# Optimization experiments

Measured on AMD Instinct MI355X. Metric: run time of the kernel, lower is better.

The kernel has to match this reference:

```python
import jax, jax.numpy as jnp
import numpy as np

B, T, C, HS = 4, 4096, 1024, 64

def setup_inputs() -> dict:
    key = jax.random.key(0)
    kx, kq, kk, kv = jax.random.split(key, 4)
    x = jax.random.normal(kx, (B, T, C), dtype=jnp.float32)
    s = 1.0 / np.sqrt(C)
    Wq = jax.random.normal(kq, (C, HS), dtype=jnp.float32) * s
    Wk = jax.random.normal(kk, (C, HS), dtype=jnp.float32) * s
    Wv = jax.random.normal(kv, (C, HS), dtype=jnp.float32) * s
    return {"x": x, "Wq": Wq, "Wk": Wk, "Wv": Wv}

def reference(x, Wq, Wk, Wv):
    # q,k,v: [B,T,HS]
    q = jnp.einsum('btc,ch->bth', x, Wq)
    k = jnp.einsum('btc,ch,->bth', x, Wk) if False else jnp.einsum('btc,ch->bth', x, Wk)
    v = jnp.einsum('btc,ch->bth', x, Wv)
    dk = q.shape[-1]
    wei = jnp.einsum('bth,bsh->bts', q, k) * (dk ** -0.5)  # [B,T,T]
    Tq = wei.shape[1]
    causal = jnp.tril(jnp.ones((Tq, Tq), dtype=bool))
    wei = jnp.where(causal, wei, -jnp.inf)
    wei = jax.nn.softmax(wei, axis=-1)
    out = jnp.einsum('bts,bsh->bth', wei, v)  # [B,T,HS]
    return out
```

## Files before the change

### kernel.cpp

```cpp
#include <hip/hip_runtime.h>
#include <stdint.h>

typedef __attribute__((ext_vector_type(8))) short short8v;
typedef __attribute__((ext_vector_type(4))) float float4v;

__device__ __forceinline__ unsigned short f32_to_bf16(float f) {
    union { float f; uint32_t u; } v; v.f = f;
    uint32_t u = v.u;
    u += 0x7FFFu + ((u >> 16) & 1u);
    return (unsigned short)(u >> 16);
}

#define T_LEN 4096
#define C_DIM 1024
#define HSZ 64

__global__ void wt_kernel(const float* __restrict__ Wq, const float* __restrict__ Wk,
                          const float* __restrict__ Wv, unsigned short* __restrict__ Wtp) {
    int idx = blockIdx.x * blockDim.x + threadIdx.x;
    int e    = idx & 7;
    int lane = (idx >> 3) & 63;
    int ks   = (idx >> 9) & 31;
    int ct   = idx >> 14;
    int g = lane >> 4, c = lane & 15;
    int k   = ks * 32 + g * 8 + e;
    int col = (ct & 3) * 16 + c;
    int m   = ct >> 2;
    const float* W = (m == 0) ? Wq : ((m == 1) ? Wk : Wv);
    Wtp[idx] = f32_to_bf16(W[(size_t)k * 64 + col]);
}

#define XCH 264

__global__ __launch_bounds__(256) void qkv_kernel(
    const float* __restrict__ x, const unsigned short* __restrict__ Wtp,
    unsigned short* __restrict__ qo, unsigned short* __restrict__ kp,
    unsigned short* __restrict__ vp)
{
    __shared__ __align__(16) unsigned short xs2[2][16 * XCH];
    const int tid = threadIdx.x;
    const int bid = (int)blockIdx.x;
    const int rowidx = (((bid >> 1) & 3) << 8) + ((bid >> 3) << 1) + (bid & 1);
    const int row0 = rowidx * 16;

    const int wave = tid >> 6, lane = tid & 63;
    const int g = lane >> 4, c = lane & 15;

    const int lrow = tid >> 6;
    float4 ld[4];

    auto LOADX = [&](int cs) {
        #pragma unroll
        for (int i = 0; i < 4; ++i) {
            int f = i * 256 + tid;
            int row = f >> 6, c4 = f & 63;
            ld[i] = *((const float4*)x + (size_t)(row0 + row) * 256 + cs * 64 + c4);
        }
    };
    auto WRITEX = [&](int buf) {
        #pragma unroll
        for (int i = 0; i < 4; ++i) {
            int f = i * 256 + tid;
            int row = f >> 6, c4 = f & 63;
            union { unsigned short s[4]; uint64_t u; } pk;
            pk.s[0] = f32_to_bf16(ld[i].x); pk.s[1] = f32_to_bf16(ld[i].y);
            pk.s[2] = f32_to_bf16(ld[i].z); pk.s[3] = f32_to_bf16(ld[i].w);
            *(uint64_t*)(&xs2[buf][row * XCH + c4 * 4]) = pk.u;
        }
    };
    (void)lrow;

    LOADX(0);
    WRITEX(0);
    __syncthreads();

    float4v acc0 = {0,0,0,0}, acc1 = {0,0,0,0}, acc2 = {0,0,0,0};
    const unsigned short* wp0 = Wtp + (size_t)((wave * 3 + 0) * 32) * 512 + lane * 8;
    const unsigned short* wp1 = Wtp + (size_t)((wave * 3 + 1) * 32) * 512 + lane * 8;
    const unsigned short* wp2 = Wtp + (size_t)((wave * 3 + 2) * 32) * 512 + lane * 8;

    for (int cs = 0; cs < 4; ++cs) {
        if (cs < 3) LOADX(cs + 1);
        const int buf = cs & 1;
        #pragma unroll
        for (int k8 = 0; k8 < 8; ++k8) {
            const int ks = cs * 8 + k8;
            short8v a  = *(const short8v*)(&xs2[buf][c * XCH + k8 * 32 + g * 8]);
            short8v b0 = *(const short8v*)(wp0 + ks * 512);
            short8v b1 = *(const short8v*)(wp1 + ks * 512);
            short8v b2 = *(const short8v*)(wp2 + ks * 512);
            acc0 = __builtin_amdgcn_mfma_f32_16x16x32_bf16(a, b0, acc0, 0, 0, 0);
            acc1 = __builtin_amdgcn_mfma_f32_16x16x32_bf16(a, b1, acc1, 0, 0, 0);
            acc2 = __builtin_amdgcn_mfma_f32_16x16x32_bf16(a, b2, acc2, 0, 0, 0);
        }
        if (cs < 3) {
            __syncthreads();
            WRITEX(buf ^ 1);
            __syncthreads();
        }
    }

    float4v accs[3] = {acc0, acc1, acc2};
    #pragma unroll
    for (int t = 0; t < 3; ++t) {
        int ct = wave * 3 + t;
        int m = ct >> 2, hcol = (ct & 3) * 16 + c;
        if (m == 2) {
            const int r0 = row0 + g * 4;
            const int b  = r0 >> 12;
            const int s0_ = r0 & 4095;
            const int t2h = s0_ >> 5;
            const int gv  = (s0_ >> 3) & 3;
            const int e0  = s0_ & 7;
            union { unsigned short s[4]; uint64_t u; } pk;
            #pragma unroll
            for (int j = 0; j < 4; ++j) pk.s[j] = f32_to_bf16(accs[t][j]);
            *(uint64_t*)(vp + (size_t)b * 262144 + t2h * 2048 + (ct & 3) * 512
                            + (gv * 16 + c) * 8 + e0) = pk.u;
        } else if (m == 1) {
            const int fbase = ((row0 & 4095) >> 6) * 8 + (((row0 & 4095) >> 4) & 3) * 2 + (hcol >> 5);
            const int b = row0 >> 12;
            unsigned short* kb = kp + (size_t)b * 262144 + (size_t)fbase * 512
                                 + (((hcol >> 3) & 3) * 16) * 8 + (hcol & 7);
            #pragma unroll
            for (int j = 0; j < 4; ++j)
                kb[(g * 4 + j) * 8] = f32_to_bf16(accs[t][j]);
        } else {
            float sc = 0.125f;
            #pragma unroll
            for (int j = 0; j < 4; ++j)
                qo[(size_t)(row0 + g * 4 + j) * 64 + hcol] = f32_to_bf16(accs[t][j] * sc);
        }
    }
}

#define PLD 72

__global__ __launch_bounds__(512) void attn_kernel(
    const unsigned short* __restrict__ qi, const unsigned short* __restrict__ kp,
    const unsigned short* __restrict__ vp, float* __restrict__ out)
{
    __shared__ __align__(16) unsigned short Ps[8][16 * PLD];
    __shared__ float CombO[6][16][64];
    __shared__ float CombM[6][16];
    __shared__ float CombL[6][16];

    const int tid   = threadIdx.x;
    const int wave  = tid >> 6, lane = tid & 63;
    const int qh    = wave & 1, slice = wave >> 1;
    const int g = lane >> 4, c = lane & 15;

    const int bid   = (int)blockIdx.x;
    const int batch = (bid >> 1) & 3;
    const int q0    = bid & 1;
    const int m_    = bid >> 3;
    const int mm    = m_ & 31;
    const int qb = q0 ? ((m_ < 32) ? 2 * mm + 1 : 126 - 2 * mm)
                      : ((m_ < 32) ? 2 * mm     : 127 - 2 * mm);

    const int rbase = qb * 32 + qh * 16;
    const size_t bo  = (size_t)batch * T_LEN * HSZ;
    const size_t bov = (size_t)batch * 262144;

    short8v qf0 = *(const short8v*)(qi + bo + (size_t)(rbase + c) * 64 +  0 + g * 8);
    short8v qf1 = *(const short8v*)(qi + bo + (size_t)(rbase + c) * 64 + 32 + g * 8);

    float4v acc[4];
    #pragma unroll
    for (int i2 = 0; i2 < 4; ++i2) acc[i2] = (float4v){0,0,0,0};
    float mrow = -3e38f;
    float lsum = 0.f;

    const int nt_w = ((rbase + 15) >> 6) + 1;
    unsigned short* Pw = &Ps[wave][0];

    short8v kf[8], kn[8];

    auto TILE = [&](int t, const short8v* kb) {
        const int s0 = t * 64;

        float4v sa[4];
        #pragma unroll
        for (int ct = 0; ct < 4; ++ct) {
            float4v z = {0, 0, 0, 0};
            z = __builtin_amdgcn_mfma_f32_16x16x32_bf16(kb[ct * 2 + 0], qf0, z, 0, 0, 0);
            sa[ct] = __builtin_amdgcn_mfma_f32_16x16x32_bf16(kb[ct * 2 + 1], qf1, z, 0, 0, 0);
        }

        short8v vf0[4];
        #pragma unroll
        for (int dt = 0; dt < 4; ++dt)
            vf0[dt] = *(const short8v*)(vp + bov + (size_t)(t * 8 + dt) * 512 + lane * 8);

        if (s0 + 63 > rbase) {
            #pragma unroll
            for (int ct = 0; ct < 4; ++ct)
                #pragma unroll
                for (int j = 0; j < 4; ++j)
                    if (s0 + ct * 16 + g * 4 + j > rbase + c) sa[ct][j] = -3e38f;
        }

        float mx01 = fmaxf(fmaxf(sa[0][0], sa[0][1]), fmaxf(sa[0][2], sa[0][3]));
        float mx11 = fmaxf(fmaxf(sa[1][0], sa[1][1]), fmaxf(sa[1][2], sa[1][3]));
        float mx21 = fmaxf(fmaxf(sa[2][0], sa[2][1]), fmaxf(sa[2][2], sa[2][3]));
        float mx31 = fmaxf(fmaxf(sa[3][0], sa[3][1]), fmaxf(sa[3][2], sa[3][3]));
        float mx = fmaxf(fmaxf(mx01, mx11), fmaxf(mx21, mx31));
        mx = fmaxf(mx, __shfl_xor(mx, 16, 64));
        mx = fmaxf(mx, __shfl_xor(mx, 32, 64));
        const float nm = fmaxf(mrow, mx);
        const float al = __expf(mrow - nm);
        mrow = nm;
        float ps = 0.f;
        #pragma unroll
        for (int ct = 0; ct < 4; ++ct)
            #pragma unroll
            for (int j = 0; j < 4; ++j) {
                float p = __expf(sa[ct][j] - nm);
                sa[ct][j] = p;
                ps += p;
            }
        lsum = lsum * al + ps;
        #pragma unroll
        for (int dt = 0; dt < 4; ++dt)
            #pragma unroll
            for (int j = 0; j < 4; ++j) acc[dt][j] *= al;

        #pragma unroll
        for (int ct = 0; ct < 4; ++ct) {
            union { unsigned short s[4]; uint64_t u; } pk4;
            #pragma unroll
            for (int j = 0; j < 4; ++j) pk4.s[j] = f32_to_bf16(sa[ct][j]);
            *(uint64_t*)(&Pw[c * PLD + ct * 16 + g * 4]) = pk4.u;
        }

        short8v vf1[4];
        #pragma unroll
        for (int dt = 0; dt < 4; ++dt)
            vf1[dt] = *(const short8v*)(vp + bov + (size_t)(t * 8 + 4 + dt) * 512 + lane * 8);

        short8v pa0 = *(const short8v*)(&Pw[c * PLD +  0 + g * 8]);
        short8v pa1 = *(const short8v*)(&Pw[c * PLD + 32 + g * 8]);

        #pragma unroll
        for (int dt = 0; dt < 4; ++dt)
            acc[dt] = __builtin_amdgcn_mfma_f32_16x16x32_bf16(vf0[dt], pa0, acc[dt], 0, 0, 0);
        #pragma unroll
        for (int dt = 0; dt < 4; ++dt)
            acc[dt] = __builtin_amdgcn_mfma_f32_16x16x32_bf16(vf1[dt], pa1, acc[dt], 0, 0, 0);
    };

    auto LOADK = [&](int t, short8v* kd) {
        #pragma unroll
        for (int f = 0; f < 8; ++f)
            kd[f] = *(const short8v*)(kp + bov + (size_t)(t * 8 + f) * 512 + lane * 8);
    };

    int t = slice;
    if (t < nt_w) {
        LOADK(t, kf);
        while (true) {
            const bool h1 = (t + 4 < nt_w);
            if (h1) LOADK(t + 4, kn);
            TILE(t, kf);
            if (!h1) break;
            t += 4;
            const bool h2 = (t + 4 < nt_w);
            if (h2) LOADK(t + 4, kf);
            TILE(t, kn);
            if (!h2) break;
            t += 4;
        }
    }

    lsum += __shfl_xor(lsum, 16, 64);
    lsum += __shfl_xor(lsum, 32, 64);

    if (slice > 0) {
        const int sidx = (slice - 1) * 2 + qh;
        #pragma unroll
        for (int dt = 0; dt < 4; ++dt)
            #pragma unroll
            for (int j = 0; j < 4; ++j)
                CombO[sidx][c][dt * 16 + g * 4 + j] = acc[dt][j];
        if (g == 0) {
            CombM[sidx][c] = mrow;
            CombL[sidx][c] = lsum;
        }
    }
    __syncthreads();

    if (slice == 0) {
        float M = mrow;
        #pragma unroll
        for (int s = 0; s < 3; ++s) M = fmaxf(M, CombM[s * 2 + qh][c]);
        const float a0 = __expf(mrow - M);
        float as[3];
        float lt = lsum * a0;
        #pragma unroll
        for (int s = 0; s < 3; ++s) {
            as[s] = __expf(CombM[s * 2 + qh][c] - M);
            lt += as[s] * CombL[s * 2 + qh][c];
        }
        const float linv = 1.0f / lt;
        #pragma unroll
        for (int dt = 0; dt < 4; ++dt) {
            float4 o;
            float* op = &o.x;
            #pragma unroll
            for (int j = 0; j < 4; ++j) {
                float v = acc[dt][j] * a0;
                #pragma unroll
                for (int s = 0; s < 3; ++s)
                    v += as[s] * CombO[s * 2 + qh][c][dt * 16 + g * 4 + j];
                op[j] = v * linv;
            }
            *(float4*)(out + bo + (size_t)(rbase + c) * 64 + dt * 16 + g * 4) = o;
        }
    }
}

extern "C" void kernel_launch(void* const* d_in, const int* in_sizes, int n_in,
                              void* d_out, int out_size, void* d_ws, size_t ws_size,
                              hipStream_t stream) {
    const float* x  = (const float*)d_in[0];
    const float* Wq = (const float*)d_in[1];
    const float* Wk = (const float*)d_in[2];
    const float* Wv = (const float*)d_in[3];

    unsigned short* Wt = (unsigned short*)d_ws;
    unsigned short* q  = (unsigned short*)((char*)d_ws + (size_t)3 * 65536 * 2);
    unsigned short* kp = q + (size_t)4 * T_LEN * HSZ;
    unsigned short* vp = kp + (size_t)4 * T_LEN * HSZ;
    float* out = (float*)d_out;

    hipLaunchKernelGGL(wt_kernel,  dim3(768), dim3(256), 0, stream, Wq, Wk, Wv, Wt);
    hipLaunchKernelGGL(qkv_kernel, dim3(1024), dim3(256), 0, stream, x, Wt, q, kp, vp);
    hipLaunchKernelGGL(attn_kernel, dim3(512), dim3(512), 0, stream, q, kp, vp, out);
}
```

Measured before the change: 57.83 us.

## Double QKV row tile per block and split K across wave halves

The QKV projection kernel now processes 32 rows per block with 512 threads instead of 16 rows with 256 threads. Each wave computes two 16-row tiles, so every weight fragment loaded is reused twice. The K dimension is split between two wave groups, and their partial sums are reduced through shared memory. This halves the grid and cuts redundant weight loads, at the cost of extra LDS, a reduction step with added barriers, and fewer blocks to spread across CUs.

```diff
diff --git a/kernel.cpp b/kernel.cpp
--- a/kernel.cpp
+++ b/kernel.cpp
@@ -32,27 +32,31 @@
 
 #define XCH 264
 
-__global__ __launch_bounds__(256) void qkv_kernel(
+__global__ __launch_bounds__(512) void qkv_kernel(
     const float* __restrict__ x, const unsigned short* __restrict__ Wtp,
     unsigned short* __restrict__ qo, unsigned short* __restrict__ kp,
     unsigned short* __restrict__ vp)
 {
-    __shared__ __align__(16) unsigned short xs2[2][16 * XCH];
+    __shared__ __align__(16) unsigned short xs2[2][32 * XCH];
+    __shared__ float part[4][2][3][64][4];
+
     const int tid = threadIdx.x;
     const int bid = (int)blockIdx.x;
-    const int rowidx = (((bid >> 1) & 3) << 8) + ((bid >> 3) << 1) + (bid & 1);
-    const int row0 = rowidx * 16;
+    const int batch = (bid >> 1) & 3;
+    const int q0    = bid & 1;
+    const int hi    = bid >> 3;
+    const int rg    = hi * 2 + q0;
+    const int row0  = batch * 4096 + rg * 32;
 
     const int wave = tid >> 6, lane = tid & 63;
+    const int wq = wave & 3, wh = wave >> 2;
     const int g = lane >> 4, c = lane & 15;
 
-    const int lrow = tid >> 6;
     float4 ld[4];
-
     auto LOADX = [&](int cs) {
         #pragma unroll
         for (int i = 0; i < 4; ++i) {
-            int f = i * 256 + tid;
+            int f = i * 512 + tid;
             int row = f >> 6, c4 = f & 63;
             ld[i] = *((const float4*)x + (size_t)(row0 + row) * 256 + cs * 64 + c4);
         }
@@ -60,7 +64,7 @@
     auto WRITEX = [&](int buf) {
         #pragma unroll
         for (int i = 0; i < 4; ++i) {
-            int f = i * 256 + tid;
+            int f = i * 512 + tid;
             int row = f >> 6, c4 = f & 63;
             union { unsigned short s[4]; uint64_t u; } pk;
             pk.s[0] = f32_to_bf16(ld[i].x); pk.s[1] = f32_to_bf16(ld[i].y);
@@ -68,30 +72,40 @@
             *(uint64_t*)(&xs2[buf][row * XCH + c4 * 4]) = pk.u;
         }
     };
-    (void)lrow;
 
     LOADX(0);
     WRITEX(0);
     __syncthreads();
 
-    float4v acc0 = {0,0,0,0}, acc1 = {0,0,0,0}, acc2 = {0,0,0,0};
-    const unsigned short* wp0 = Wtp + (size_t)((wave * 3 + 0) * 32) * 512 + lane * 8;
-    const unsigned short* wp1 = Wtp + (size_t)((wave * 3 + 1) * 32) * 512 + lane * 8;
-    const unsigned short* wp2 = Wtp + (size_t)((wave * 3 + 2) * 32) * 512 + lane * 8;
+    float4v acc[2][3];
+    #pragma unroll
+    for (int rt = 0; rt < 2; ++rt)
+        #pragma unroll
+        for (int t = 0; t < 3; ++t) acc[rt][t] = (float4v){0,0,0,0};
+
+    const unsigned short* wp0 = Wtp + (size_t)((wq * 3 + 0) * 32) * 512 + lane * 8;
+    const unsigned short* wp1 = Wtp + (size_t)((wq * 3 + 1) * 32) * 512 + lane * 8;
+    const unsigned short* wp2 = Wtp + (size_t)((wq * 3 + 2) * 32) * 512 + lane * 8;
 
     for (int cs = 0; cs < 4; ++cs) {
         if (cs < 3) LOADX(cs + 1);
         const int buf = cs & 1;
         #pragma unroll
-        for (int k8 = 0; k8 < 8; ++k8) {
-            const int ks = cs * 8 + k8;
-            short8v a  = *(const short8v*)(&xs2[buf][c * XCH + k8 * 32 + g * 8]);
-            short8v b0 = *(const short8v*)(wp0 + ks * 512);
-            short8v b1 = *(const short8v*)(wp1 + ks * 512);
-            short8v b2 = *(const short8v*)(wp2 + ks * 512);
-            acc0 = __builtin_amdgcn_mfma_f32_16x16x32_bf16(a, b0, acc0, 0, 0, 0);
-            acc1 = __builtin_amdgcn_mfma_f32_16x16x32_bf16(a, b1, acc1, 0, 0, 0);
-            acc2 = __builtin_amdgcn_mfma_f32_16x16x32_bf16(a, b2, acc2, 0, 0, 0);
+        for (int ksi = 0; ksi < 4; ++ksi) {
+            const int kc = 2 * ksi + wh;
+            const int ks = cs * 8 + kc;
+            const int koff = kc * 32 + g * 8;
+            short8v a0 = *(const short8v*)(&xs2[buf][(0 * 16 + c) * XCH + koff]);
+            short8v a1 = *(const short8v*)(&xs2[buf][(1 * 16 + c) * XCH + koff]);
+            short8v b0 = *(const short8v*)(wp0 + (size_t)ks * 512);
+            short8v b1 = *(const short8v*)(wp1 + (size_t)ks * 512);
+            short8v b2 = *(const short8v*)(wp2 + (size_t)ks * 512);
+            acc[0][0] = __builtin_amdgcn_mfma_f32_16x16x32_bf16(a0, b0, acc[0][0], 0, 0, 0);
+            acc[0][1] = __builtin_amdgcn_mfma_f32_16x16x32_bf16(a0, b1, acc[0][1], 0, 0, 0);
+            acc[0][2] = __builtin_amdgcn_mfma_f32_16x16x32_bf16(a0, b2, acc[0][2], 0, 0, 0);
+            acc[1][0] = __builtin_amdgcn_mfma_f32_16x16x32_bf16(a1, b0, acc[1][0], 0, 0, 0);
+            acc[1][1] = __builtin_amdgcn_mfma_f32_16x16x32_bf16(a1, b1, acc[1][1], 0, 0, 0);
+            acc[1][2] = __builtin_amdgcn_mfma_f32_16x16x32_bf16(a1, b2, acc[1][2], 0, 0, 0);
         }
         if (cs < 3) {
             __syncthreads();
@@ -100,36 +114,55 @@
         }
     }
 
-    float4v accs[3] = {acc0, acc1, acc2};
-    #pragma unroll
-    for (int t = 0; t < 3; ++t) {
-        int ct = wave * 3 + t;
-        int m = ct >> 2, hcol = (ct & 3) * 16 + c;
-        if (m == 2) {
-            const int r0 = row0 + g * 4;
-            const int b  = r0 >> 12;
-            const int s0_ = r0 & 4095;
-            const int t2h = s0_ >> 5;
-            const int gv  = (s0_ >> 3) & 3;
-            const int e0  = s0_ & 7;
-            union { unsigned short s[4]; uint64_t u; } pk;
-            #pragma unroll
-            for (int j = 0; j < 4; ++j) pk.s[j] = f32_to_bf16(accs[t][j]);
-            *(uint64_t*)(vp + (size_t)b * 262144 + t2h * 2048 + (ct & 3) * 512
-                            + (gv * 16 + c) * 8 + e0) = pk.u;
-        } else if (m == 1) {
-            const int fbase = ((row0 & 4095) >> 6) * 8 + (((row0 & 4095) >> 4) & 3) * 2 + (hcol >> 5);
-            const int b = row0 >> 12;
-            unsigned short* kb = kp + (size_t)b * 262144 + (size_t)fbase * 512
-                                 + (((hcol >> 3) & 3) * 16) * 8 + (hcol & 7);
-            #pragma unroll
-            for (int j = 0; j < 4; ++j)
-                kb[(g * 4 + j) * 8] = f32_to_bf16(accs[t][j]);
-        } else {
-            float sc = 0.125f;
-            #pragma unroll
-            for (int j = 0; j < 4; ++j)
-                qo[(size_t)(row0 + g * 4 + j) * 64 + hcol] = f32_to_bf16(accs[t][j] * sc);
+    __syncthreads();
+    if (wh == 1) {
+        #pragma unroll
+        for (int rt = 0; rt < 2; ++rt)
+            #pragma unroll
+            for (int t = 0; t < 3; ++t)
+                #pragma unroll
+                for (int j = 0; j < 4; ++j)
+                    part[wq][rt][t][lane][j] = acc[rt][t][j];
+    }
+    __syncthreads();
+    if (wh == 0) {
+        #pragma unroll
+        for (int rt = 0; rt < 2; ++rt) {
+            const int row0t = row0 + rt * 16;
+            #pragma unroll
+            for (int t = 0; t < 3; ++t) {
+                float4v av = acc[rt][t];
+                #pragma unroll
+                for (int j = 0; j < 4; ++j) av[j] += part[wq][rt][t][lane][j];
+                int ct = wq * 3 + t;
+                int m = ct >> 2, hcol = (ct & 3) * 16 + c;
+                if (m == 2) {
+                    const int r0 = row0t + g * 4;
+                    const int b  = r0 >> 12;
+                    const int s0_ = r0 & 4095;
+                    const int t2h = s0_ >> 5;
+                    const int gv  = (s0_ >> 3) & 3;
+                    const int e0  = s0_ & 7;
+                    union { unsigned short s[4]; uint64_t u; } pk;
+                    #pragma unroll
+                    for (int j = 0; j < 4; ++j) pk.s[j] = f32_to_bf16(av[j]);
+                    *(uint64_t*)(vp + (size_t)b * 262144 + t2h * 2048 + (ct & 3) * 512
+                                    + (gv * 16 + c) * 8 + e0) = pk.u;
+                } else if (m == 1) {
+                    const int fbase = ((row0t & 4095) >> 6) * 8 + (((row0t & 4095) >> 4) & 3) * 2 + (hcol >> 5);
+                    const int b = row0t >> 12;
+                    unsigned short* kb = kp + (size_t)b * 262144 + (size_t)fbase * 512
+                                         + (((hcol >> 3) & 3) * 16) * 8 + (hcol & 7);
+                    #pragma unroll
+                    for (int j = 0; j < 4; ++j)
+                        kb[(g * 4 + j) * 8] = f32_to_bf16(av[j]);
+                } else {
+                    float sc = 0.125f;
+                    #pragma unroll
+                    for (int j = 0; j < 4; ++j)
+                        qo[(size_t)(row0t + g * 4 + j) * 64 + hcol] = f32_to_bf16(av[j] * sc);
+                }
+            }
         }
     }
 }
@@ -334,6 +367,6 @@
     float* out = (float*)d_out;
 
     hipLaunchKernelGGL(wt_kernel,  dim3(768), dim3(256), 0, stream, Wq, Wk, Wv, Wt);
-    hipLaunchKernelGGL(qkv_kernel, dim3(1024), dim3(256), 0, stream, x, Wt, q, kp, vp);
+    hipLaunchKernelGGL(qkv_kernel, dim3(512), dim3(512), 0, stream, x, Wt, q, kp, vp);
     hipLaunchKernelGGL(attn_kernel, dim3(512), dim3(512), 0, stream, q, kp, vp, out);
 }
```

Measured after the change: 52.86 us. -8.6%, faster.
